# Kernel tuning notes

Hardware: AMD Instinct MI355X
Metric: run time of the kernel (lower is better)

The kernel has to match this reference:

```python
import jax, jax.numpy as jnp
import numpy as np

NODE_F = 8      # node_features
HID = 128       # hidden_dim
HEADS = 8       # nn.MultiheadAttention num_heads
OUT = 256       # output_dim
MAX_ATOMS = 4096  # max_pocket_atoms
NEIGHBOR_RADIUS = 3.0   # _compute_surface_scores neighbor_radius


def setup_inputs() -> dict:
    key = jax.random.key(0)
    ks = jax.random.split(key, 16)
    N, M = 16384, 32
    x = jax.random.normal(ks[0], (N, NODE_F), dtype=jnp.float32)
    pos = jax.random.normal(ks[1], (N, 3), dtype=jnp.float32) * 10.0
    ligand_pos = jax.random.normal(ks[2], (M, 3), dtype=jnp.float32) * 3.0

    def lin(k, fan_in, fan_out):
        return jax.random.normal(k, (fan_in, fan_out), dtype=jnp.float32) / np.sqrt(fan_in)

    return {
        'x': x, 'pos': pos, 'ligand_pos': ligand_pos,
        'W_node': lin(ks[3], NODE_F, HID), 'b_node': jnp.zeros((HID,), jnp.float32),
        'Wq': lin(ks[4], HID, HID), 'bq': jnp.zeros((HID,), jnp.float32),
        'Wk': lin(ks[5], HID, HID), 'bk': jnp.zeros((HID,), jnp.float32),
        'Wv': lin(ks[6], HID, HID), 'bv': jnp.zeros((HID,), jnp.float32),
        'Wo': lin(ks[7], HID, HID), 'bo': jnp.zeros((HID,), jnp.float32),
        'W1': lin(ks[8], HID, OUT), 'b1': jnp.zeros((OUT,), jnp.float32),
        'W2': lin(ks[9], OUT, OUT), 'b2': jnp.zeros((OUT,), jnp.float32),
    }


def _select_binding_site(pos, ligand_pos, k):
    # select_by_binding_site_proximity: distance-to-ligand-center + surface scores, topk
    lig_center = jnp.mean(ligand_pos, axis=0)                       # [3]
    d_lig = jnp.linalg.norm(pos - lig_center, axis=1)               # [N]
    # _compute_surface_scores: cdist(pos,pos) < 3.0, count neighbors (minus self)
    sq = jnp.sum(pos * pos, axis=1)                                 # [N]
    d2 = sq[:, None] + sq[None, :] - 2.0 * (pos @ pos.T)            # [N,N] squared distances
    neighbor_counts = jnp.sum(d2 < NEIGHBOR_RADIUS ** 2, axis=1) - 1
    surface = 1.0 / (neighbor_counts.astype(jnp.float32) + 1.0)
    scores = 1.0 / (1.0 + d_lig / 5.0) + 0.5 * surface
    _, idx = jax.lax.top_k(scores, k)                               # largest=True
    return idx


def reference(x, pos, ligand_pos, W_node, b_node, Wq, bq, Wk, bk, Wv, bv, Wo, bo, W1, b1, W2, b2):
    # N > max_pocket_atoms -> smart selection (adaptive with ligand_pos => binding_site)
    idx = _select_binding_site(pos, ligand_pos, MAX_ATOMS)
    xs = x[idx]                                                     # [K, NODE_F]

    # node embedding (E3 net call fails in the original -> h = node_embedding(x))
    h = xs @ W_node + b_node                                        # [K, HID]

    # MultiheadAttention over the single (batch=None) sequence, eval mode (no dropout)
    K = MAX_ATOMS
    dh = HID // HEADS
    q = (h @ Wq + bq).reshape(K, HEADS, dh).transpose(1, 0, 2)      # [H,K,dh]
    k_ = (h @ Wk + bk).reshape(K, HEADS, dh).transpose(1, 0, 2)
    v = (h @ Wv + bv).reshape(K, HEADS, dh).transpose(1, 0, 2)
    attn = jax.nn.softmax(jnp.einsum('hqd,hkd->hqk', q, k_) / np.sqrt(dh), axis=-1)
    av = jnp.einsum('hqk,hkd->hqd', attn, v).transpose(1, 0, 2).reshape(K, HID)
    h_att = av @ Wo + bo                                            # [K, HID]

    # global mean pool + output projection (Linear-ReLU-Linear)
    pooled = jnp.mean(h_att, axis=0)                                # [HID]
    out = jax.nn.relu(pooled @ W1 + b1) @ W2 + b2                   # [OUT]
    return out
```

## Files before the change

kernel.cpp:

```cpp
#include <hip/hip_runtime.h>
#include <cstdint>
#include <cstddef>

#define NPTS 16384
#define KSEL 4096
#define HIDDEN 128
#define NHEADS 8
#define DHEAD 16
#define OUTD 256
#define NSLICE 4
#define FCAP 131072
#define LCAP 512
#define TAU 0.2f

typedef __attribute__((ext_vector_type(8))) short bf16x8;
typedef __attribute__((ext_vector_type(4))) float f32x4;
typedef __attribute__((ext_vector_type(16))) float f32x16;

#if defined(__has_builtin)
#if __has_builtin(__builtin_amdgcn_exp2f)
#define E2(x) __builtin_amdgcn_exp2f(x)
#endif
#endif
#ifndef E2
#define E2(x) exp2f(x)
#endif

constexpr size_t OFF_PA    = 1024;
constexpr size_t OFF_PB    = OFF_PA  + (size_t)NPTS*32;
constexpr size_t OFF_SQ    = OFF_PB  + (size_t)NPTS*32;
constexpr size_t OFF_DL    = OFF_SQ  + (size_t)NPTS*4;
constexpr size_t OFF_CNT   = OFF_DL  + (size_t)NPTS*4;
constexpr size_t OFF_NFLAG = OFF_CNT + (size_t)NPTS*4;
constexpr size_t OFF_FLG   = OFF_NFLAG + 1024;
constexpr size_t OFF_SEL   = OFF_FLG + (size_t)FCAP*4;
constexpr size_t SZ_PK     = (size_t)NHEADS*KSEL*32*2;
constexpr size_t OFF_QPK   = OFF_SEL + (size_t)KSEL*4;
constexpr size_t OFF_KPK   = OFF_QPK + SZ_PK;
constexpr size_t OFF_V     = OFF_KPK + SZ_PK;
constexpr size_t OFF_LP    = OFF_V  + (size_t)KSEL*HIDDEN*4;
constexpr size_t OFF_RL    = OFF_LP + (size_t)NHEADS*KSEL*NSLICE*4;
constexpr size_t OFF_WP    = OFF_RL + (size_t)NHEADS*KSEL*4;
constexpr size_t OFF_PAV   = OFF_WP + (size_t)NHEADS*KSEL*NSLICE*4;

__device__ __forceinline__ unsigned short f2bf(float f) {
    union { float f; unsigned u; } v; v.f = f;
    unsigned r = v.u + 0x7fffu + ((v.u >> 16) & 1u);
    return (unsigned short)(r >> 16);
}
__device__ __forceinline__ float bf2f(unsigned short h) {
    union { unsigned u; float f; } v; v.u = ((unsigned)h) << 16;
    return v.f;
}

__global__ void __launch_bounds__(256) k_prep(const float* __restrict__ pos, const float* __restrict__ lig, int M,
                       unsigned short* __restrict__ pa, unsigned short* __restrict__ pb,
                       float* __restrict__ sq, float* __restrict__ dl, float* __restrict__ pav) {
    __shared__ float ls[128];
    __shared__ float ctr[3];
    int tid = threadIdx.x;
    if (blockIdx.x == 0 && tid < HIDDEN) pav[tid] = 0.f;
    for (int i = tid; i < 3 * M; i += 256) ls[i] = lig[i];
    __syncthreads();
    if (tid < 3) {
        float s = 0.f;
        for (int i = 0; i < M; i++) s += ls[i * 3 + tid];
        ctr[tid] = s / (float)M;
    }
    __syncthreads();
    int i = blockIdx.x * 256 + tid;
    float x = pos[i*3+0], y = pos[i*3+1], z = pos[i*3+2];
    float s = (x*x + y*y) + z*z;
    sq[i] = s;
    float dx = x - ctr[0], dy = y - ctr[1], dz = z - ctr[2];
    dl[i] = sqrtf((dx*dx + dy*dy) + dz*dz);
    unsigned short xh = f2bf(x); float xr = bf2f(xh); float xl = x - xr;
    unsigned short yh = f2bf(y); float yr = bf2f(yh); float yl = y - yr;
    unsigned short zh = f2bf(z); float zr = bf2f(zh); float zl = z - zr;
    unsigned short xlb = f2bf(xl), ylb = f2bf(yl), zlb = f2bf(zl);
    unsigned short xhA = f2bf(-2.f*xr), xlA = f2bf(-2.f*xl);
    unsigned short yhA = f2bf(-2.f*yr), ylA = f2bf(-2.f*yl);
    unsigned short zhA = f2bf(-2.f*zr), zlA = f2bf(-2.f*zl);
    float sm9 = s - 9.0f;
    unsigned short sihA = f2bf(sm9);
    unsigned short silA = f2bf(sm9 - bf2f(sihA));
    unsigned short sih = f2bf(s);
    unsigned short sil = f2bf(s - bf2f(sih));
    unsigned short one = f2bf(1.0f);
    union { unsigned short s[16]; float4 f[2]; } A, B;
    A.s[0]=xhA; A.s[1]=xhA; A.s[2]=xlA;
    A.s[3]=yhA; A.s[4]=yhA; A.s[5]=ylA;
    A.s[6]=zhA; A.s[7]=zhA; A.s[8]=zlA;
    A.s[9]=xlA; A.s[10]=ylA; A.s[11]=zlA;
    A.s[12]=sihA; A.s[13]=silA; A.s[14]=one; A.s[15]=one;
    B.s[0]=xh;  B.s[1]=xlb;  B.s[2]=xh;
    B.s[3]=yh;  B.s[4]=ylb;  B.s[5]=yh;
    B.s[6]=zh;  B.s[7]=zlb;  B.s[8]=zh;
    B.s[9]=xlb; B.s[10]=ylb; B.s[11]=zlb;
    B.s[12]=one; B.s[13]=one; B.s[14]=sih; B.s[15]=sil;
    float4* pad = (float4*)(pa + (size_t)i * 16);
    pad[0] = A.f[0]; pad[1] = A.f[1];
    float4* pbd = (float4*)(pb + (size_t)i * 16);
    pbd[0] = B.f[0]; pbd[1] = B.f[1];
}

__global__ void __launch_bounds__(256) k_neighbor(
        const unsigned short* __restrict__ pa, const unsigned short* __restrict__ pb,
        int* __restrict__ cnt, unsigned int* __restrict__ flg, unsigned int* __restrict__ nflag) {
    __shared__ unsigned short js[256 * 24];
    __shared__ unsigned int fbuf[LCAP];
    __shared__ unsigned int fcnt, fbase;
    int tid = threadIdx.x;
    if (tid == 0) fcnt = 0;
    int lane = tid & 63, w = tid >> 6;
    int half = lane >> 5, il = lane & 31;
    int i = blockIdx.x * 128 + w * 32 + il;
    bf16x8 bfrag = *(const bf16x8*)(pb + (size_t)i * 16 + half * 8);
    int jb0 = blockIdx.y * 1024;
    int acc = 0;
    const f32x16 czero = {0.f,0.f,0.f,0.f,0.f,0.f,0.f,0.f,0.f,0.f,0.f,0.f,0.f,0.f,0.f,0.f};
    for (int chv = 0; chv < 4; chv++) {
        int jb = jb0 + chv * 256;
        __syncthreads();
        {
            const float4* src = (const float4*)(pa + (size_t)(jb + tid) * 16);
            float4 v0 = src[0], v1 = src[1];
            float4* dst = (float4*)&js[tid * 24];
            dst[0] = v0; dst[1] = v1;
        }
        __syncthreads();
        #pragma unroll 2
        for (int t = 0; t < 8; t++) {
            bf16x8 afrag = *(const bf16x8*)&js[(t * 32 + il) * 24 + half * 8];
            f32x16 c = __builtin_amdgcn_mfma_f32_32x32x16_bf16(afrag, bfrag, czero, 0, 0, 0);
            int cs = 0;
            #pragma unroll
            for (int r = 0; r < 16; r++) cs += (c[r] < -TAU);
            acc += cs;
            float a0 = fminf(fabsf(c[0]),  fabsf(c[1]));
            float a1 = fminf(fabsf(c[2]),  fabsf(c[3]));
            float a2 = fminf(fabsf(c[4]),  fabsf(c[5]));
            float a3 = fminf(fabsf(c[6]),  fabsf(c[7]));
            float a4 = fminf(fabsf(c[8]),  fabsf(c[9]));
            float a5 = fminf(fabsf(c[10]), fabsf(c[11]));
            float a6 = fminf(fabsf(c[12]), fabsf(c[13]));
            float a7 = fminf(fabsf(c[14]), fabsf(c[15]));
            float b0 = fminf(a0, a1), b1 = fminf(a2, a3);
            float b2 = fminf(a4, a5), b3 = fminf(a6, a7);
            float mn = fminf(fminf(b0, b1), fminf(b2, b3));
            if (mn <= TAU) {
                int jt = jb + t * 32;
                #pragma unroll
                for (int r = 0; r < 16; r++) {
                    float d = c[r];
                    if (d >= -TAU && d < TAU) {
                        int j = jt + (r & 3) + 8 * (r >> 2) + 4 * half;
                        unsigned xx = atomicAdd(&fcnt, 1u);
                        if (xx < LCAP) fbuf[xx] = ((unsigned)i << 14) | (unsigned)j;
                    }
                }
            }
        }
    }
    acc += __shfl_xor(acc, 32);
    if (half == 0) atomicAdd(&cnt[i], acc);
    __syncthreads();
    if (tid == 0) {
        unsigned cf = fcnt; if (cf > LCAP) cf = LCAP;
        fcnt = cf;
        fbase = atomicAdd(nflag, cf);
    }
    __syncthreads();
    unsigned cf = fcnt, fb = fbase;
    for (unsigned xx = tid; xx < cf; xx += 256) {
        unsigned di = fb + xx;
        if (di < FCAP) flg[di] = fbuf[xx];
    }
}

__global__ void __launch_bounds__(256) k_fixup(const float* __restrict__ pos, const float* __restrict__ sq,
        const unsigned int* __restrict__ flg, const unsigned int* __restrict__ nflag,
        int* __restrict__ cnt) {
    int nf = (int)*nflag; if (nf > FCAP) nf = FCAP;
    for (int idx = blockIdx.x * 256 + threadIdx.x; idx < nf; idx += gridDim.x * 256) {
        unsigned pr = flg[idx];
        int i = (int)((pr >> 14) & 16383u), j = (int)(pr & 16383u);
        float xi = pos[i*3+0], yi = pos[i*3+1], zi = pos[i*3+2];
        float xj = pos[j*3+0], yj = pos[j*3+1], zj = pos[j*3+2];
        float dot = fmaf(xi, xj, fmaf(yi, yj, zi * zj));
        float d2 = (sq[i] + sq[j]) - 2.0f * dot;
        if (d2 < 9.0f) atomicAdd(&cnt[i], 1);
    }
}

__global__ void __launch_bounds__(1024) k_select(const float* __restrict__ dl, const int* __restrict__ cnt,
                                                 int* __restrict__ sel) {
    __shared__ unsigned int sk[NPTS];
    __shared__ int hist[256];
    __shared__ int scan2[256];
    __shared__ unsigned int s_prefix;
    __shared__ int s_rem, s_eqtot, s_nout, s_digit, s_cgt;
    int tid = threadIdx.x;
    for (int i = tid; i < NPTS; i += 1024) {
        float score = 1.0f / (1.0f + dl[i] / 5.0f) + 0.5f * (1.0f / (float)cnt[i]);
        unsigned int u = __float_as_uint(score);
        sk[i] = u ^ ((u & 0x80000000u) ? 0xFFFFFFFFu : 0x80000000u);
    }
    if (tid == 0) { s_prefix = 0; s_rem = KSEL; s_nout = 0; s_eqtot = 0; }
    __syncthreads();
    for (int p = 0; p < 4; p++) {
        int sh = 24 - 8 * p;
        if (tid < 256) hist[tid] = 0;
        __syncthreads();
        unsigned int pref = s_prefix;
        int shp = (p == 0) ? 0 : (32 - 8 * p);
        for (int i = tid; i < NPTS; i += 1024) {
            unsigned int key = sk[i];
            bool m = (p == 0) || ((key >> shp) == pref);
            if (m) atomicAdd(&hist[(key >> sh) & 255], 1);
        }
        __syncthreads();
        if (tid < 256) scan2[tid] = hist[tid];
        __syncthreads();
        for (int off = 1; off < 256; off <<= 1) {
            int v = 0;
            if (tid < 256) { v = scan2[tid]; if (tid + off < 256) v += scan2[tid + off]; }
            __syncthreads();
            if (tid < 256) scan2[tid] = v;
            __syncthreads();
        }
        int rem = s_rem;
        if (tid < 256) {
            int hi = scan2[tid];
            int lo = hi - hist[tid];
            if (hi >= rem && lo < rem) { s_digit = tid; s_cgt = lo; }
        }
        __syncthreads();
        if (tid == 0) {
            s_prefix = (s_prefix << 8) | (unsigned int)s_digit;
            s_rem = rem - s_cgt;
            if (p == 3) s_eqtot = hist[s_digit];
        }
        __syncthreads();
    }
    unsigned int T = s_prefix;
    int need_eq = s_rem;
    for (int i = tid; i < NPTS; i += 1024)
        if (sk[i] > T) sel[atomicAdd(&s_nout, 1)] = i;
    __syncthreads();
    if (s_eqtot == need_eq) {
        for (int i = tid; i < NPTS; i += 1024)
            if (sk[i] == T) sel[atomicAdd(&s_nout, 1)] = i;
    } else {
        for (int i = tid; i < NPTS; i += 1024) {
            if (sk[i] == T) {
                int rank = 0;
                for (int j = 0; j < i; j++) rank += (sk[j] == T);
                if (rank < need_eq) sel[atomicAdd(&s_nout, 1)] = i;
            }
        }
    }
}

__device__ __forceinline__ void proj4(const float hs[4][HIDDEN], const float* __restrict__ W,
                                      float b, int d, float* acc) {
    #pragma unroll
    for (int r = 0; r < 4; r++) acc[r] = b;
    for (int c = 0; c < HIDDEN; c += 4) {
        float w0 = W[(c+0)*HIDDEN+d], w1 = W[(c+1)*HIDDEN+d], w2 = W[(c+2)*HIDDEN+d], w3 = W[(c+3)*HIDDEN+d];
        #pragma unroll
        for (int r = 0; r < 4; r++) {
            float4 h4 = *(const float4*)&hs[r][c];
            float a = acc[r];
            a = fmaf(h4.x, w0, a); a = fmaf(h4.y, w1, a); a = fmaf(h4.z, w2, a); a = fmaf(h4.w, w3, a);
            acc[r] = a;
        }
    }
}

__global__ void __launch_bounds__(128) k_qkv(const float* __restrict__ x, const int* __restrict__ sel,
        const float* __restrict__ Wn, const float* __restrict__ bn,
        const float* __restrict__ Wq, const float* __restrict__ bq,
        const float* __restrict__ Wk, const float* __restrict__ bk,
        const float* __restrict__ Wv, const float* __restrict__ bv,
        unsigned short* __restrict__ qpk, unsigned short* __restrict__ kpk,
        float* __restrict__ vg) {
    __shared__ float xs[4][8];
    __shared__ __align__(16) float hs[4][HIDDEN];
    int d = threadIdx.x;
    int r0 = blockIdx.x * 4;
    if (d < 32) { int rr = d >> 3, cc = d & 7; xs[rr][cc] = x[(size_t)sel[r0 + rr] * 8 + cc]; }
    __syncthreads();
    {
        float wn[8];
        #pragma unroll
        for (int c = 0; c < 8; c++) wn[c] = Wn[c * HIDDEN + d];
        float b = bn[d];
        #pragma unroll
        for (int r = 0; r < 4; r++) {
            float a = b;
            #pragma unroll
            for (int c = 0; c < 8; c++) a = fmaf(xs[r][c], wn[c], a);
            hs[r][d] = a;
        }
    }
    __syncthreads();
    int hh = d >> 4, dd = d & 15;
    float acc[4];
    proj4(hs, Wq, bq[d], d, acc);
    #pragma unroll
    for (int r = 0; r < 4; r++) {
        float val = acc[r] * 0.36067376022224085f;
        unsigned short hi = f2bf(val);
        unsigned short lo = f2bf(val - bf2f(hi));
        size_t idx = ((size_t)(hh * KSEL) + r0 + r) * 32 + dd;
        qpk[idx] = hi; qpk[idx + 16] = lo;
    }
    proj4(hs, Wk, bk[d], d, acc);
    #pragma unroll
    for (int r = 0; r < 4; r++) {
        float val = acc[r];
        unsigned short hi = f2bf(val);
        unsigned short lo = f2bf(val - bf2f(hi));
        size_t idx = ((size_t)(hh * KSEL) + r0 + r) * 32 + dd;
        kpk[idx] = hi; kpk[idx + 16] = lo;
    }
    proj4(hs, Wv, bv[d], d, acc);
    #pragma unroll
    for (int r = 0; r < 4; r++) vg[(size_t)(r0+r)*HIDDEN + d] = acc[r];
}

__global__ void __launch_bounds__(512) k_attn_l(
        const unsigned short* __restrict__ qpk, const unsigned short* __restrict__ kpk,
        float* __restrict__ lp) {
    __shared__ unsigned short smem[256 * 40];
    int tid = threadIdx.x;
    int ks = blockIdx.x, yg = blockIdx.y, h = blockIdx.z;
    size_t hb = (size_t)h * KSEL;
    int lane = tid & 63, w = tid >> 6;
    int n = lane & 15, g = lane >> 4;
    int q0w = yg * 128 + w * 16;
    bf16x8 afrag = *(const bf16x8*)(qpk + (hb + q0w + n) * 32 + g * 8);
    float l0 = 0.f, l1 = 0.f, l2 = 0.f, l3 = 0.f;
    int b1off = (g & 1) * 8;
    int b2off = 16 + g * 8;
    for (int kc = 0; kc < 4; kc++) {
        __syncthreads();
        {
            int row = tid >> 1, hf = tid & 1;
            int krow = ks * 1024 + kc * 256 + row;
            const float4* src = (const float4*)(kpk + (hb + krow) * 32 + hf * 16);
            float4 a0 = src[0], a1 = src[1];
            float4* dst = (float4*)&smem[row * 40 + hf * 16];
            dst[0] = a0; dst[1] = a1;
        }
        __syncthreads();
        #pragma unroll 4
        for (int t = 0; t < 16; t++) {
            const unsigned short* rowp = &smem[(t * 16 + n) * 40];
            bf16x8 b1 = *(const bf16x8*)(rowp + b1off);
            bf16x8 b2 = {0,0,0,0,0,0,0,0};
            if (g < 2) b2 = *(const bf16x8*)(rowp + b2off);
            f32x4 c = {0.f, 0.f, 0.f, 0.f};
            c = __builtin_amdgcn_mfma_f32_16x16x32_bf16(afrag, b1, c, 0, 0, 0);
            c = __builtin_amdgcn_mfma_f32_16x16x32_bf16(afrag, b2, c, 0, 0, 0);
            l0 += E2(c[0]); l1 += E2(c[1]); l2 += E2(c[2]); l3 += E2(c[3]);
        }
    }
    #pragma unroll
    for (int m = 1; m < 16; m <<= 1) {
        l0 += __shfl_xor(l0, m); l1 += __shfl_xor(l1, m);
        l2 += __shfl_xor(l2, m); l3 += __shfl_xor(l3, m);
    }
    if (n == 0) {
        size_t base = (hb + q0w + g * 4) * NSLICE + ks;
        lp[base]            = l0; lp[base + NSLICE]     = l1;
        lp[base + 2*NSLICE] = l2; lp[base + 3*NSLICE]   = l3;
    }
}

__global__ void __launch_bounds__(512) k_attn_w(
        const unsigned short* __restrict__ qpk, const unsigned short* __restrict__ kpk,
        const float* __restrict__ lp, float* __restrict__ wp) {
    __shared__ unsigned short smem[256 * 40];
    __shared__ float rls[256];
    int tid = threadIdx.x;
    int qs = blockIdx.x, yg = blockIdx.y, h = blockIdx.z;
    size_t hb = (size_t)h * KSEL;
    int lane = tid & 63, w = tid >> 6;
    int n = lane & 15, g = lane >> 4;
    int j0w = yg * 128 + w * 16;
    bf16x8 afrag = *(const bf16x8*)(kpk + (hb + j0w + n) * 32 + g * 8);
    float w0 = 0.f, w1 = 0.f, w2 = 0.f, w3 = 0.f;
    int b1off = (g & 1) * 8;
    int b2off = 16 + g * 8;
    for (int qc = 0; qc < 4; qc++) {
        __syncthreads();
        {
            int row = tid >> 1, hf = tid & 1;
            int qrow = qs * 1024 + qc * 256 + row;
            const float4* src = (const float4*)(qpk + (hb + qrow) * 32 + hf * 16);
            float4 a0 = src[0], a1 = src[1];
            float4* dst = (float4*)&smem[row * 40 + hf * 16];
            dst[0] = a0; dst[1] = a1;
            if (hf == 0) {
                float4 p = ((const float4*)lp)[hb + qrow];
                rls[row] = 1.0f / ((p.x + p.y) + (p.z + p.w));
            }
        }
        __syncthreads();
        #pragma unroll 4
        for (int t = 0; t < 16; t++) {
            const unsigned short* rowp = &smem[(t * 16 + n) * 40];
            bf16x8 b1 = *(const bf16x8*)(rowp + b1off);
            bf16x8 b2 = {0,0,0,0,0,0,0,0};
            if (g < 2) b2 = *(const bf16x8*)(rowp + b2off);
            f32x4 c = {0.f, 0.f, 0.f, 0.f};
            c = __builtin_amdgcn_mfma_f32_16x16x32_bf16(afrag, b1, c, 0, 0, 0);
            c = __builtin_amdgcn_mfma_f32_16x16x32_bf16(afrag, b2, c, 0, 0, 0);
            float rv = rls[t * 16 + n];
            w0 = fmaf(E2(c[0]), rv, w0); w1 = fmaf(E2(c[1]), rv, w1);
            w2 = fmaf(E2(c[2]), rv, w2); w3 = fmaf(E2(c[3]), rv, w3);
        }
    }
    #pragma unroll
    for (int m = 1; m < 16; m <<= 1) {
        w0 += __shfl_xor(w0, m); w1 += __shfl_xor(w1, m);
        w2 += __shfl_xor(w2, m); w3 += __shfl_xor(w3, m);
    }
    if (n == 0) {
        size_t base = (hb + j0w + g * 4) * NSLICE + qs;
        wp[base]            = w0; wp[base + NSLICE]     = w1;
        wp[base + 2*NSLICE] = w2; wp[base + 3*NSLICE]   = w3;
    }
}

__global__ void __launch_bounds__(256) k_colsum(const float* __restrict__ wp, const float* __restrict__ vg,
                                                float* __restrict__ pav) {
    __shared__ float wl[NHEADS][32];
    __shared__ float red[128];
    int tid = threadIdx.x;
    int j0 = blockIdx.x * 32;
    {
        int h = tid >> 5, jl = tid & 31;
        float4 p = ((const float4*)wp)[(size_t)h * KSEL + j0 + jl];
        wl[h][jl] = (p.x + p.y) + (p.z + p.w);
    }
    __syncthreads();
    int d = tid & 127, g = tid >> 7;
    int h = d >> 4;
    float acc = 0.f;
    for (int jl = g * 16; jl < g * 16 + 16; jl++)
        acc = fmaf(wl[h][jl], vg[(size_t)(j0 + jl) * HIDDEN + d], acc);
    if (g == 1) red[d] = acc;
    __syncthreads();
    if (g == 0) atomicAdd(&pav[d], (acc + red[d]) * (1.0f / (float)KSEL));
}

__global__ void __launch_bounds__(256) k_final(const float* __restrict__ pav,
        const float* __restrict__ Wo, const float* __restrict__ bo,
        const float* __restrict__ W1, const float* __restrict__ b1,
        const float* __restrict__ W2, const float* __restrict__ b2,
        float* __restrict__ out) {
    __shared__ float sp[HIDDEN];
    __shared__ float st[OUTD];
    int t = threadIdx.x;
    if (t < HIDDEN) {
        float a = bo[t];
        for (int c = 0; c < HIDDEN; c++) a = fmaf(pav[c], Wo[c * HIDDEN + t], a);
        sp[t] = a;
    }
    __syncthreads();
    {
        float a = b1[t];
        for (int c = 0; c < HIDDEN; c++) a = fmaf(sp[c], W1[c * OUTD + t], a);
        st[t] = fmaxf(a, 0.f);
    }
    __syncthreads();
    {
        float o = b2[t];
        for (int c = 0; c < OUTD; c++) o = fmaf(st[c], W2[c * OUTD + t], o);
        out[t] = o;
    }
}

extern "C" void kernel_launch(void* const* d_in, const int* in_sizes, int n_in,
                              void* d_out, int out_size, void* d_ws, size_t ws_size,
                              hipStream_t stream) {
    (void)n_in; (void)out_size; (void)ws_size;
    const float* x   = (const float*)d_in[0];
    const float* pos = (const float*)d_in[1];
    const float* lig = (const float*)d_in[2];
    const float* Wn  = (const float*)d_in[3];
    const float* bn  = (const float*)d_in[4];
    const float* Wq  = (const float*)d_in[5];
    const float* bq  = (const float*)d_in[6];
    const float* Wk  = (const float*)d_in[7];
    const float* bk  = (const float*)d_in[8];
    const float* Wv  = (const float*)d_in[9];
    const float* bv  = (const float*)d_in[10];
    const float* Wo  = (const float*)d_in[11];
    const float* bo  = (const float*)d_in[12];
    const float* W1  = (const float*)d_in[13];
    const float* b1  = (const float*)d_in[14];
    const float* W2  = (const float*)d_in[15];
    const float* b2  = (const float*)d_in[16];
    int M = in_sizes[2] / 3;

    char* ws = (char*)d_ws;
    unsigned short* pa  = (unsigned short*)(ws + OFF_PA);
    unsigned short* pb  = (unsigned short*)(ws + OFF_PB);
    float*          sq  = (float*)(ws + OFF_SQ);
    float*          dl  = (float*)(ws + OFF_DL);
    int*            cnt = (int*)  (ws + OFF_CNT);
    unsigned int*   nfl = (unsigned int*)(ws + OFF_NFLAG);
    unsigned int*   flg = (unsigned int*)(ws + OFF_FLG);
    int*            sel = (int*)  (ws + OFF_SEL);
    unsigned short* qpk = (unsigned short*)(ws + OFF_QPK);
    unsigned short* kpk = (unsigned short*)(ws + OFF_KPK);
    float*          vg  = (float*)(ws + OFF_V);
    float*          lp  = (float*)(ws + OFF_LP);
    float*          wp  = (float*)(ws + OFF_WP);
    float*          pav = (float*)(ws + OFF_PAV);

    hipMemsetAsync(ws + OFF_CNT, 0, (size_t)NPTS * 4 + 1024, stream);

    hipLaunchKernelGGL(k_prep,     dim3(64),       dim3(256),  0, stream, pos, lig, M, pa, pb, sq, dl, pav);
    hipLaunchKernelGGL(k_neighbor, dim3(128, 16),  dim3(256),  0, stream, pa, pb, cnt, flg, nfl);
    hipLaunchKernelGGL(k_fixup,    dim3(32),       dim3(256),  0, stream, pos, sq, flg, nfl, cnt);
    hipLaunchKernelGGL(k_select,   dim3(1),        dim3(1024), 0, stream, dl, cnt, sel);
    hipLaunchKernelGGL(k_qkv,      dim3(KSEL/4),   dim3(128),  0, stream, x, sel, Wn, bn, Wq, bq, Wk, bk, Wv, bv, qpk, kpk, vg);
    hipLaunchKernelGGL(k_attn_l,   dim3(4, 32, 8), dim3(512),  0, stream, qpk, kpk, lp);
    hipLaunchKernelGGL(k_attn_w,   dim3(4, 32, 8), dim3(512),  0, stream, qpk, kpk, lp, wp);
    hipLaunchKernelGGL(k_colsum,   dim3(KSEL/32),  dim3(256),  0, stream, wp, vg, pav);
    hipLaunchKernelGGL(k_final,    dim3(1),        dim3(256),  0, stream, pav, Wo, bo, W1, b1, W2, b2, (float*)d_out);
}
```

Baseline: 258.6 us.

## Exploit symmetry of pairwise neighbor counts to compute only upper-triangle tiles

The neighbor-count kernel now launches only the block tiles on or above the diagonal (1088 instead of 2048) and masks the lower part of diagonal-straddling tiles. Each tile's bitmask of close pairs is staged in shared memory and column-summed, so the j-side counts are added with atomics, and the fixup kernel increments both i and j. Self-pairs are excluded, so the score uses cnt+1. This roughly halves the MFMA distance work, but adds a shared-memory mask transpose, extra global atomics, and a longer index-mapping prologue.

```diff
diff --git a/kernel.cpp b/kernel.cpp
--- a/kernel.cpp
+++ b/kernel.cpp
@@ -108,15 +108,23 @@
         const unsigned short* __restrict__ pa, const unsigned short* __restrict__ pb,
         int* __restrict__ cnt, unsigned int* __restrict__ flg, unsigned int* __restrict__ nflag) {
     __shared__ unsigned short js[256 * 24];
+    __shared__ unsigned short msk[128][64];
     __shared__ unsigned int fbuf[LCAP];
     __shared__ unsigned int fcnt, fbase;
     int tid = threadIdx.x;
     if (tid == 0) fcnt = 0;
+    int bid = blockIdx.x;
+    int g = 0, base = 0;
+    while (bid >= base + 8 * (16 - g)) { base += 8 * (16 - g); g++; }
+    int local = bid - base, ng = 16 - g;
+    int bi = 8 * g + local / ng;
+    int bj = g + local % ng;
+    bool straddle = (bj == g);
     int lane = tid & 63, w = tid >> 6;
     int half = lane >> 5, il = lane & 31;
-    int i = blockIdx.x * 128 + w * 32 + il;
+    int i = bi * 128 + w * 32 + il;
     bf16x8 bfrag = *(const bf16x8*)(pb + (size_t)i * 16 + half * 8);
-    int jb0 = blockIdx.y * 1024;
+    int jb0 = bj * 1024;
     int acc = 0;
     const f32x16 czero = {0.f,0.f,0.f,0.f,0.f,0.f,0.f,0.f,0.f,0.f,0.f,0.f,0.f,0.f,0.f,0.f};
     for (int chv = 0; chv < 4; chv++) {
@@ -133,10 +141,23 @@
         for (int t = 0; t < 8; t++) {
             bf16x8 afrag = *(const bf16x8*)&js[(t * 32 + il) * 24 + half * 8];
             f32x16 c = __builtin_amdgcn_mfma_f32_32x32x16_bf16(afrag, bfrag, czero, 0, 0, 0);
-            int cs = 0;
+            int jt4 = jb + t * 32 + 4 * half;
+            unsigned jm = 0xFFFFu;
+            if (straddle) {
+                int lim = i - jt4;
+                jm = 0;
+                #pragma unroll
+                for (int r = 15; r >= 0; r--) {
+                    int sb = (r & 3) + 8 * (r >> 2);
+                    jm = (jm << 1) | (unsigned)(sb > lim);
+                }
+            }
+            unsigned cm = 0;
             #pragma unroll
-            for (int r = 0; r < 16; r++) cs += (c[r] < -TAU);
-            acc += cs;
+            for (int r = 15; r >= 0; r--) cm = (cm << 1) | (unsigned)(c[r] < -TAU);
+            cm &= jm;
+            acc += __builtin_popcount(cm);
+            msk[w * 32 + chv * 8 + t][lane] = (unsigned short)cm;
             float a0 = fminf(fabsf(c[0]),  fabsf(c[1]));
             float a1 = fminf(fabsf(c[2]),  fabsf(c[3]));
             float a2 = fminf(fabsf(c[4]),  fabsf(c[5]));
@@ -149,12 +170,11 @@
             float b2 = fminf(a4, a5), b3 = fminf(a6, a7);
             float mn = fminf(fminf(b0, b1), fminf(b2, b3));
             if (mn <= TAU) {
-                int jt = jb + t * 32;
                 #pragma unroll
                 for (int r = 0; r < 16; r++) {
                     float d = c[r];
-                    if (d >= -TAU && d < TAU) {
-                        int j = jt + (r & 3) + 8 * (r >> 2) + 4 * half;
+                    if (d >= -TAU && d < TAU && ((jm >> r) & 1u)) {
+                        int j = jt4 + (r & 3) + 8 * (r >> 2);
                         unsigned xx = atomicAdd(&fcnt, 1u);
                         if (xx < LCAP) fbuf[xx] = ((unsigned)i << 14) | (unsigned)j;
                     }
@@ -169,6 +189,25 @@
         unsigned cf = fcnt; if (cf > LCAP) cf = LCAP;
         fcnt = cf;
         fbase = atomicAdd(nflag, cf);
+    }
+    #pragma unroll
+    for (int q = 0; q < 4; q++) {
+        int jl = q * 256 + tid;
+        int chv = jl >> 8, v = jl & 255, t = v >> 5, s = v & 31;
+        int r = (s & 3) | ((s >> 3) << 2);
+        int h = (s >> 2) & 1;
+        int row = chv * 8 + t;
+        int total = 0;
+        #pragma unroll
+        for (int w2 = 0; w2 < 4; w2++) {
+            const unsigned int* mp = (const unsigned int*)&msk[w2 * 32 + row][h * 32];
+            #pragma unroll
+            for (int u = 0; u < 16; u++) {
+                unsigned int m2 = mp[u];
+                total += (int)((m2 >> r) & 1u) + (int)((m2 >> (16 + r)) & 1u);
+            }
+        }
+        if (total) atomicAdd(&cnt[jb0 + jl], total);
     }
     __syncthreads();
     unsigned cf = fcnt, fb = fbase;
@@ -189,7 +228,7 @@
         float xj = pos[j*3+0], yj = pos[j*3+1], zj = pos[j*3+2];
         float dot = fmaf(xi, xj, fmaf(yi, yj, zi * zj));
         float d2 = (sq[i] + sq[j]) - 2.0f * dot;
-        if (d2 < 9.0f) atomicAdd(&cnt[i], 1);
+        if (d2 < 9.0f) { atomicAdd(&cnt[i], 1); atomicAdd(&cnt[j], 1); }
     }
 }
 
@@ -202,7 +241,7 @@
     __shared__ int s_rem, s_eqtot, s_nout, s_digit, s_cgt;
     int tid = threadIdx.x;
     for (int i = tid; i < NPTS; i += 1024) {
-        float score = 1.0f / (1.0f + dl[i] / 5.0f) + 0.5f * (1.0f / (float)cnt[i]);
+        float score = 1.0f / (1.0f + dl[i] / 5.0f) + 0.5f / (float)(cnt[i] + 1);
         unsigned int u = __float_as_uint(score);
         sk[i] = u ^ ((u & 0x80000000u) ? 0xFFFFFFFFu : 0x80000000u);
     }
@@ -526,7 +565,7 @@
     hipMemsetAsync(ws + OFF_CNT, 0, (size_t)NPTS * 4 + 1024, stream);
 
     hipLaunchKernelGGL(k_prep,     dim3(64),       dim3(256),  0, stream, pos, lig, M, pa, pb, sq, dl, pav);
-    hipLaunchKernelGGL(k_neighbor, dim3(128, 16),  dim3(256),  0, stream, pa, pb, cnt, flg, nfl);
+    hipLaunchKernelGGL(k_neighbor, dim3(1088),     dim3(256),  0, stream, pa, pb, cnt, flg, nfl);
     hipLaunchKernelGGL(k_fixup,    dim3(32),       dim3(256),  0, stream, pos, sq, flg, nfl, cnt);
     hipLaunchKernelGGL(k_select,   dim3(1),        dim3(1024), 0, stream, dl, cnt, sel);
     hipLaunchKernelGGL(k_qkv,      dim3(KSEL/4),   dim3(128),  0, stream, x, sel, Wn, bn, Wq, bq, Wk, bk, Wv, bv, qpk, kpk, vg);
```

Result: slower. 265.1 us (+2.5%).
